# Kernel tuning notes

Measured on AMD Instinct MI355X. Metric: run time of the kernel, lower is better.

Reference implementation:

```python
import jax, jax.numpy as jnp
import numpy as np

B, T, P, D = 8, 2048, 4, 768

def setup_inputs() -> dict:
    key = jax.random.key(0)
    k1, k2, k3 = jax.random.split(key, 3)
    text_inputs = jax.random.normal(k1, (B, T, D), dtype=jnp.float32)
    sit_mask = jax.random.randint(k2, (B, T), 0, 2).astype(jnp.float32)
    proposition_matrix = jax.random.normal(k3, (B, T, P, D), dtype=jnp.float32)
    return {"text_inputs": text_inputs, "sit_mask": sit_mask, "proposition_matrix": proposition_matrix}

def reference(text_inputs, sit_mask, proposition_matrix):
    # D from proposition_matrix (matches text hidden dim), used for softmax scaling
    d = proposition_matrix.shape[-1]
    t = text_inputs.shape[1]
    # raw scores [B,T,T], scaled by 1/sqrt(D)
    scores = jnp.einsum('bid,bjd->bij', text_inputs, text_inputs) * (1.0 / jnp.sqrt(jnp.asarray(d, text_inputs.dtype)))
    # causal mask: strictly upper triangular -> -inf (tokens attend to self + past)
    causal = jnp.tril(jnp.ones((t, t), dtype=bool))  # [T,T]
    scores = jnp.where(causal[None, :, :], scores, -jnp.inf)
    weights = jax.nn.softmax(scores, axis=2)
    # padding mask via outer product of sit_mask; zero AFTER softmax (no renorm), as in original
    pad = (sit_mask[:, :, None] * sit_mask[:, None, :]) != 0  # [B,T,T]
    weights = jnp.where(pad, weights, jnp.zeros((), weights.dtype))
    out = jnp.einsum('bij,bjd->bid', weights, text_inputs)  # [B,T,D]
    # concat_self_hidden=True
    out = jnp.concatenate([out, text_inputs], axis=-1)  # [B,T,2D]
    return out
```

## Files before the change

kernel.cpp:

```cpp
#include <hip/hip_runtime.h>
#include <math.h>

constexpr int kT = 2048;
constexpr int kD = 768;
constexpr int kTileShorts = 16 * kD;
constexpr int kTilesPerBatch = kT / 16;

typedef __attribute__((ext_vector_type(8))) short short8;
typedef __attribute__((ext_vector_type(4))) float f32x4;
typedef __attribute__((ext_vector_type(16))) float f32x16;

#define FB(f) __builtin_bit_cast(unsigned, (f))
__device__ __forceinline__ unsigned pk_hi16(unsigned hi, unsigned lo) {
  return __builtin_amdgcn_perm(hi, lo, 0x07060302);
}
__device__ __forceinline__ unsigned pk_lo16(unsigned hi, unsigned lo) {
  return __builtin_amdgcn_perm(hi, lo, 0x05040100);
}

__device__ __forceinline__ void lds_barrier() {
  asm volatile("" ::: "memory");
  __builtin_amdgcn_s_waitcnt(0xC07F);
  __builtin_amdgcn_s_barrier();
  asm volatile("" ::: "memory");
}

__device__ __forceinline__ void gload_lds16(const void* g, void* l) {
  __builtin_amdgcn_global_load_lds(
      (const __attribute__((address_space(1))) unsigned int*)g,
      (__attribute__((address_space(3))) unsigned int*)l, 16, 0, 0);
}

__global__ __launch_bounds__(256) void prep_bf16(
    const float* __restrict__ x,
    unsigned short* __restrict__ xbf, unsigned short* __restrict__ xvt)
{
  const int tid = threadIdx.x;
  const int w = tid >> 6, l = tid & 63;
  const int l15 = l & 15, q4 = l >> 4;
  const int bt = (int)blockIdx.x;
  const float* xb = x + (size_t)bt * 16 * kD;
  unsigned short* ob = xbf + (size_t)bt * kTileShorts;
  unsigned short* ov = xvt + (size_t)bt * kTileShorts;

#pragma unroll
  for (int it = 0; it < 3; ++it) {
    const int dq = l15 + 16 * it + 48 * w;
    unsigned lo[4], hi[4];
#pragma unroll
    for (int jj = 0; jj < 4; ++jj) {
      const float4 f = *(const float4*)(xb + (size_t)(q4 + 4 * jj) * kD + 4 * dq);
      lo[jj] = pk_hi16(FB(f.y), FB(f.x));
      hi[jj] = pk_hi16(FB(f.w), FB(f.z));
    }
    const int dp = 4 * (l15 + 16 * it);
    const int g = dp >> 3, e0 = dp & 7;
#pragma unroll
    for (int jj = 0; jj < 4; ++jj) {
      const int j = q4 + 4 * jj;
      uint2 v; v.x = lo[jj]; v.y = hi[jj];
      *(uint2*)&ob[w * 3072 + j * 192 + ((g ^ (j & 7)) << 3) + e0] = v;
    }
    const int jb = (4 * q4) ^ (8 * ((dq >> 2) & 1));
    const int base = dq * 64 + jb;
    uint2 v;
    v.x = pk_lo16(lo[1], lo[0]); v.y = pk_lo16(lo[3], lo[2]);
    *(uint2*)&ov[base + ((0 ^ (dq & 3)) << 4)] = v;
    v.x = pk_hi16(lo[1], lo[0]); v.y = pk_hi16(lo[3], lo[2]);
    *(uint2*)&ov[base + ((1 ^ (dq & 3)) << 4)] = v;
    v.x = pk_lo16(hi[1], hi[0]); v.y = pk_lo16(hi[3], hi[2]);
    *(uint2*)&ov[base + ((2 ^ (dq & 3)) << 4)] = v;
    v.x = pk_hi16(hi[1], hi[0]); v.y = pk_hi16(hi[3], hi[2]);
    *(uint2*)&ov[base + ((3 ^ (dq & 3)) << 4)] = v;
  }
}

__global__ __launch_bounds__(256, 2) void attn_mfma4(
    const float* __restrict__ x, const float* __restrict__ mask,
    const unsigned short* __restrict__ xbf,
    const unsigned short* __restrict__ xvt,
    float* __restrict__ out)
{
  const int tid = threadIdx.x;
  const int w = tid >> 6, l = tid & 63;
  const int l15 = l & 15, q4 = l >> 4;
  const int l31 = l & 31, h2 = l >> 5;

  const int bid = (int)blockIdx.x;
  const int b = bid & 7;
  const int s = bid >> 3;
  const int qq = (s < 32) ? (63 - s) : (s - 32);
  const int i0 = qq << 5;

  const float* xb = x + (size_t)b * kT * kD;
  const float* mrow = mask + (size_t)b * kT;
  const unsigned short* xbfB = xbf + (size_t)b * kTilesPerBatch * kTileShorts;
  const unsigned short* xvtB = xvt + (size_t)b * kTilesPerBatch * kTileShorts;

  __shared__ unsigned short xKc[12288];
  __shared__ unsigned short VTb[12288];
  __shared__ float sPart[2][4][16][36];
  __shared__ unsigned short Pm[2][32][16];
  __shared__ float corrS[2][32];
  __shared__ float invlS[32];
  __shared__ float msk[kT];

  {
    const char* msrc = (const char*)mrow + 2048 * w;
    char* mdst = (char*)&msk[512 * w];
    gload_lds16(msrc + 16 * l, mdst);
    gload_lds16(msrc + 1024 + 16 * l, mdst + 1024);
  }

  short8 qf[2][6];
#pragma unroll
  for (int mt = 0; mt < 2; ++mt) {
    const int tq = (i0 >> 4) + mt;
    const unsigned short* tp = xbfB + (size_t)tq * kTileShorts + w * 3072 + l15 * 192;
#pragma unroll
    for (int s6 = 0; s6 < 6; ++s6)
      qf[mt][s6] = *(const short8*)&tp[((4 * s6 + q4) ^ (l15 & 7)) << 3];
  }

  f32x16 o[6];
#pragma unroll
  for (int nt = 0; nt < 6; ++nt)
#pragma unroll
    for (int e = 0; e < 16; ++e) o[nt][e] = 0.0f;

  float mrun = -INFINITY, lrun = 0.0f;
  const float scale = 0.036084391824351615f;
  const int nTiles = i0 / 16 + 2;

  const int q = tid & 7, sr = tid >> 3;
  const int jA = (q >> 1) + 8 * (q & 1);
  const int irow = i0 + sr;

  const int D0 = 48 * w + (l31 >> 2);
  const int vtb_off0 = D0 * 64 + (((l31 & 3) ^ (D0 & 3)) << 4)
                     + ((8 * h2) ^ (8 * ((l31 >> 4) & 1)));

  auto stageK = [&](int t) {
    const unsigned short* src = xbfB + (size_t)t * kTileShorts + w * 3072 + 8 * l;
    unsigned short* dst = &xKc[w * 3072];
#pragma unroll
    for (int i = 0; i < 6; ++i) gload_lds16(src + 512 * i, dst + 512 * i);
  };
  auto stageV = [&](int t) {
    const unsigned short* src = xvtB + (size_t)t * kTileShorts + w * 3072 + 8 * l;
    unsigned short* dst = &VTb[w * 3072];
#pragma unroll
    for (int i = 0; i < 6; ++i) gload_lds16(src + 512 * i, dst + 512 * i);
  };

  stageK(0);
  stageV(0);
  asm volatile("s_waitcnt vmcnt(12)" ::: "memory");
  lds_barrier();

  for (int t = 0; t < nTiles; ++t) {
    const int par = t & 1;
    const int j0 = t << 4;

    asm volatile("s_waitcnt vmcnt(6)" ::: "memory");

    {
      f32x4 sf0, sf1;
#pragma unroll
      for (int e = 0; e < 4; ++e) { sf0[e] = 0.f; sf1[e] = 0.f; }
      const unsigned short* kbase = &xKc[w * 3072 + l15 * 192];
#pragma unroll
      for (int s6 = 0; s6 < 6; ++s6) {
        short8 kb = *(const short8*)&kbase[((4 * s6 + q4) ^ (l15 & 7)) << 3];
        sf0 = __builtin_amdgcn_mfma_f32_16x16x32_bf16(qf[0][s6], kb, sf0, 0, 0, 0);
        sf1 = __builtin_amdgcn_mfma_f32_16x16x32_bf16(qf[1][s6], kb, sf1, 0, 0, 0);
      }
      *(f32x4*)&sPart[par][w][l15][4 * q4]      = sf0;
      *(f32x4*)&sPart[par][w][l15][16 + 4 * q4] = sf1;
    }

    if (t + 1 < nTiles) {
      asm volatile("s_waitcnt lgkmcnt(0)" ::: "memory");
      stageK(t + 1);
    }
    lds_barrier();

    {
      float s0 = 0.f, s1 = 0.f;
#pragma unroll
      for (int ww = 0; ww < 4; ++ww) {
        s0 += sPart[par][ww][jA][sr];
        s1 += sPart[par][ww][jA + 4][sr];
      }
      const float mskA = msk[j0 + jA];
      const float mskB = msk[j0 + jA + 4];
      const int ja = j0 + jA, jb_ = j0 + jA + 4;
      float a0 = (ja  <= irow) ? s0 * scale : -INFINITY;
      float a1 = (jb_ <= irow) ? s1 * scale : -INFINITY;
      float loc = fmaxf(a0, a1);
      loc = fmaxf(loc, __shfl_xor(loc, 1, 64));
      loc = fmaxf(loc, __shfl_xor(loc, 2, 64));
      loc = fmaxf(loc, __shfl_xor(loc, 4, 64));
      const float mn = fmaxf(mrun, loc);
      const float corr = __expf(mrun - mn);
      const float p0 = __expf(a0 - mn);
      const float p1 = __expf(a1 - mn);
      float rs = p0 + p1;
      rs += __shfl_xor(rs, 1, 64);
      rs += __shfl_xor(rs, 2, 64);
      rs += __shfl_xor(rs, 4, 64);
      lrun = lrun * corr + rs;
      mrun = mn;
      const float w0 = (mskA != 0.f) ? p0 : 0.f;
      const float w1 = (mskB != 0.f) ? p1 : 0.f;
      *(unsigned*)&Pm[par][sr][2 * q] = pk_hi16(FB(w1), FB(w0));
      if (q == 0) corrS[par][sr] = corr;
    }
    lds_barrier();

    if (t + 1 < nTiles) { asm volatile("s_waitcnt vmcnt(6)" ::: "memory"); }
    else                { asm volatile("s_waitcnt vmcnt(0)" ::: "memory"); }

    {
      float cr[16];
#pragma unroll
      for (int e4 = 0; e4 < 4; ++e4) {
        f32x4 qd = *(const f32x4*)&corrS[par][8 * e4 + 4 * h2];
#pragma unroll
        for (int ee = 0; ee < 4; ++ee) cr[4 * e4 + ee] = qd[ee];
      }
#pragma unroll
      for (int nt = 0; nt < 6; ++nt)
#pragma unroll
        for (int e = 0; e < 16; ++e) o[nt][e] *= cr[e];
      short8 pa = *(const short8*)&Pm[par][l31][8 * h2];
#pragma unroll
      for (int nt = 0; nt < 6; ++nt) {
        short8 vb = *(const short8*)&VTb[vtb_off0 + 512 * nt];
        o[nt] = __builtin_amdgcn_mfma_f32_32x32x16_bf16(pa, vb, o[nt], 0, 0, 0);
      }
    }

    if (t + 1 < nTiles) {
      asm volatile("s_waitcnt lgkmcnt(0)" ::: "memory");
      stageV(t + 1);
    }
  }

  if (q == 0) invlS[sr] = (msk[irow] != 0.f) ? 1.0f / lrun : 0.0f;
  lds_barrier();
  {
    float il[16];
#pragma unroll
    for (int e4 = 0; e4 < 4; ++e4) {
      f32x4 qd = *(const f32x4*)&invlS[8 * e4 + 4 * h2];
#pragma unroll
      for (int ee = 0; ee < 4; ++ee) il[4 * e4 + ee] = qd[ee];
    }
    float* ob = out + (size_t)(b * kT + i0) * (2 * kD);
#pragma unroll
    for (int nt = 0; nt < 6; ++nt) {
      const int col = 192 * w + 32 * nt + l31;
#pragma unroll
      for (int e = 0; e < 16; ++e) {
        const int row = (e & 3) + 8 * (e >> 2) + 4 * h2;
        ob[(size_t)row * (2 * kD) + col] = o[nt][e] * il[e];
      }
    }
#pragma unroll
    for (int pass = 0; pass < 2; ++pass) {
      const int rr = (tid >> 4) + 16 * pass;
      const float* srcr = xb + (size_t)(i0 + rr) * kD;
      float* dstr = ob + (size_t)rr * (2 * kD) + kD;
#pragma unroll
      for (int it = 0; it < 12; ++it) {
        const int d4 = (tid & 15) + 16 * it;
        *(float4*)(dstr + 4 * d4) = *(const float4*)(srcr + 4 * d4);
      }
    }
  }
}

extern "C" void kernel_launch(void* const* d_in, const int* in_sizes, int n_in,
                              void* d_out, int out_size, void* d_ws, size_t ws_size,
                              hipStream_t stream) {
  const float* x    = (const float*)d_in[0];
  const float* mask = (const float*)d_in[1];
  float* out = (float*)d_out;
  unsigned short* xbf = (unsigned short*)d_ws;
  unsigned short* xvt = xbf + (size_t)8 * kTilesPerBatch * kTileShorts;
  prep_bf16<<<dim3(8 * kTilesPerBatch), dim3(256), 0, stream>>>(x, xbf, xvt);
  attn_mfma4<<<dim3(512), dim3(256), 0, stream>>>(x, mask, xbf, xvt, out);
}
```

Baseline: 462.4 us.

## Split heavy causal query blocks across two KV halves with combine kernel

The 32 heaviest query blocks per batch (the second half of the sequence) are each split into two blocks covering halves of the key range. Each half writes unnormalized partial outputs into the output buffer (second half into the concat slot) and saves its running max and sum to workspace. A new combine kernel merges the halves using log-sum-exp rescaling and then writes the self-hidden concat. The grid grows from 512 to 768 blocks, aiming to balance load and shorten the critical path, at the cost of an extra launch and a read-modify-write of the heavy rows.

```diff
diff --git a/kernel.cpp b/kernel.cpp
--- a/kernel.cpp
+++ b/kernel.cpp
@@ -75,11 +75,11 @@
   }
 }
 
-__global__ __launch_bounds__(256, 2) void attn_mfma4(
+__global__ __launch_bounds__(256, 2) void attn_mfma5(
     const float* __restrict__ x, const float* __restrict__ mask,
     const unsigned short* __restrict__ xbf,
     const unsigned short* __restrict__ xvt,
-    float* __restrict__ out)
+    float* __restrict__ out, float* __restrict__ ml)
 {
   const int tid = threadIdx.x;
   const int w = tid >> 6, l = tid & 63;
@@ -89,7 +89,27 @@
   const int bid = (int)blockIdx.x;
   const int b = bid & 7;
   const int s = bid >> 3;
-  const int qq = (s < 32) ? (63 - s) : (s - 32);
+  int qq, t0, t1, mode;
+  if (s < 80) {
+    int g = (s * 2) / 5;
+    if (g > 31) g = 31;
+    while (g < 31 && (2 * (g + 1) + ((g + 2) >> 1)) <= s) ++g;
+    while (g > 0 && (2 * g + ((g + 1) >> 1)) > s) --g;
+    const int r = s - (2 * g + ((g + 1) >> 1));
+    if (r < 2) {
+      qq = 63 - g;
+      const int H = qq + 1;
+      mode = 1 + r;
+      t0 = (r == 0) ? 0 : H;
+      t1 = (r == 0) ? H : 2 * H;
+    } else {
+      qq = 31 - (g >> 1);
+      mode = 0; t0 = 0; t1 = 2 * qq + 2;
+    }
+  } else {
+    qq = 15 - (s - 80);
+    mode = 0; t0 = 0; t1 = 2 * qq + 2;
+  }
   const int i0 = qq << 5;
 
   const float* xb = x + (size_t)b * kT * kD;
@@ -130,7 +150,6 @@
 
   float mrun = -INFINITY, lrun = 0.0f;
   const float scale = 0.036084391824351615f;
-  const int nTiles = i0 / 16 + 2;
 
   const int q = tid & 7, sr = tid >> 3;
   const int jA = (q >> 1) + 8 * (q & 1);
@@ -153,12 +172,12 @@
     for (int i = 0; i < 6; ++i) gload_lds16(src + 512 * i, dst + 512 * i);
   };
 
-  stageK(0);
-  stageV(0);
+  stageK(t0);
+  stageV(t0);
   asm volatile("s_waitcnt vmcnt(12)" ::: "memory");
   lds_barrier();
 
-  for (int t = 0; t < nTiles; ++t) {
+  for (int t = t0; t < t1; ++t) {
     const int par = t & 1;
     const int j0 = t << 4;
 
@@ -179,7 +198,7 @@
       *(f32x4*)&sPart[par][w][l15][16 + 4 * q4] = sf1;
     }
 
-    if (t + 1 < nTiles) {
+    if (t + 1 < t1) {
       asm volatile("s_waitcnt lgkmcnt(0)" ::: "memory");
       stageK(t + 1);
     }
@@ -218,8 +237,8 @@
     }
     lds_barrier();
 
-    if (t + 1 < nTiles) { asm volatile("s_waitcnt vmcnt(6)" ::: "memory"); }
-    else                { asm volatile("s_waitcnt vmcnt(0)" ::: "memory"); }
+    if (t + 1 < t1) { asm volatile("s_waitcnt vmcnt(6)" ::: "memory"); }
+    else            { asm volatile("s_waitcnt vmcnt(0)" ::: "memory"); }
 
     {
       float cr[16];
@@ -241,15 +260,15 @@
       }
     }
 
-    if (t + 1 < nTiles) {
+    if (t + 1 < t1) {
       asm volatile("s_waitcnt lgkmcnt(0)" ::: "memory");
       stageV(t + 1);
     }
   }
 
-  if (q == 0) invlS[sr] = (msk[irow] != 0.f) ? 1.0f / lrun : 0.0f;
-  lds_barrier();
-  {
+  if (mode == 0) {
+    if (q == 0) invlS[sr] = (msk[irow] != 0.f) ? 1.0f / lrun : 0.0f;
+    lds_barrier();
     float il[16];
 #pragma unroll
     for (int e4 = 0; e4 < 4; ++e4) {
@@ -277,6 +296,60 @@
         const int d4 = (tid & 15) + 16 * it;
         *(float4*)(dstr + 4 * d4) = *(const float4*)(srcr + 4 * d4);
       }
+    }
+  } else {
+    float* ob = out + (size_t)(b * kT + i0) * (2 * kD) + ((mode == 2) ? kD : 0);
+#pragma unroll
+    for (int nt = 0; nt < 6; ++nt) {
+      const int col = 192 * w + 32 * nt + l31;
+#pragma unroll
+      for (int e = 0; e < 16; ++e) {
+        const int row = (e & 3) + 8 * (e >> 2) + 4 * h2;
+        ob[(size_t)row * (2 * kD) + col] = o[nt][e];
+      }
+    }
+    if (q == 0) {
+      const int base = (((b * 32 + (qq - 32)) * 2 + (mode - 1)) * 64);
+      ml[base + sr]      = mrun;
+      ml[base + 32 + sr] = lrun;
+    }
+  }
+}
+
+__global__ __launch_bounds__(256) void combine_heavy(
+    const float* __restrict__ x, const float* __restrict__ mask,
+    const float* __restrict__ ml, float* __restrict__ out)
+{
+  const int tid = threadIdx.x;
+  const int bid = (int)blockIdx.x;
+  const int b = bid & 7;
+  const int hq = bid >> 3;
+  const int i0 = (hq + 32) << 5;
+  const float* mrow = mask + (size_t)b * kT;
+  const float* mlq = ml + (((size_t)b * 32 + hq) * 2) * 64;
+
+  for (int r = 0; r < 32; ++r) {
+    const int i = i0 + r;
+    float* orow = out + (size_t)(b * kT + i) * (2 * kD);
+    const float* xrow = x + (size_t)(b * kT + i) * kD;
+    const float m1 = mlq[r],      l1 = mlq[32 + r];
+    const float m2 = mlq[64 + r], l2 = mlq[96 + r];
+    const float m = fmaxf(m1, m2);
+    const float al = __expf(m1 - m), be = __expf(m2 - m);
+    const float lsum = al * l1 + be * l2;
+    const float gate = (mrow[i] != 0.f) ? 1.0f / lsum : 0.0f;
+    const float ga = gate * al, gb = gate * be;
+    if (tid < 192) {
+      float4 o1 = *(const float4*)(orow + 4 * tid);
+      float4 o2 = *(const float4*)(orow + kD + 4 * tid);
+      float4 xv = *(const float4*)(xrow + 4 * tid);
+      float4 fo;
+      fo.x = ga * o1.x + gb * o2.x;
+      fo.y = ga * o1.y + gb * o2.y;
+      fo.z = ga * o1.z + gb * o2.z;
+      fo.w = ga * o1.w + gb * o2.w;
+      *(float4*)(orow + 4 * tid) = fo;
+      *(float4*)(orow + kD + 4 * tid) = xv;
     }
   }
 }
@@ -289,6 +362,8 @@
   float* out = (float*)d_out;
   unsigned short* xbf = (unsigned short*)d_ws;
   unsigned short* xvt = xbf + (size_t)8 * kTilesPerBatch * kTileShorts;
+  float* ml = (float*)(xvt + (size_t)8 * kTilesPerBatch * kTileShorts);
   prep_bf16<<<dim3(8 * kTilesPerBatch), dim3(256), 0, stream>>>(x, xbf, xvt);
-  attn_mfma4<<<dim3(512), dim3(256), 0, stream>>>(x, mask, xbf, xvt, out);
-}
+  attn_mfma5<<<dim3(768), dim3(256), 0, stream>>>(x, mask, xbf, xvt, out, ml);
+  combine_heavy<<<dim3(256), dim3(256), 0, stream>>>(x, mask, ml, out);
+}
```

Result: faster. 446.3 us (-3.5%).
